# Kernel optimization log

Measured on AMD Instinct MI355X. Metric: run time of the kernel, lower is better.

The kernel has to match this reference:

```python
import jax, jax.numpy as jnp
import numpy as np

B, N = 2, 8192
FUN, EMB = 7, 3
H = 512
HEADS = 8
DH = H // HEADS  # 64
G = 32           # slice_num
L = 4            # n_layers
OUT = 4
MLP_H = 4 * H


def _ln(x, g, b, eps=1e-5):
    m = x.mean(-1, keepdims=True)
    v = ((x - m) ** 2).mean(-1, keepdims=True)
    return (x - m) * jax.lax.rsqrt(v + eps) * g + b


def _forward(fun, emb, W_pre1, b_pre1, W_pre2, b_pre2, placeholder,
             ln1_g, ln1_b, Wfx, bfx, Wx, bx, Wslice, bslice, temp,
             Wq, Wk, Wv, Wo, bo, ln2_g, ln2_b, Wm1, bm1, Wm2, bm2,
             lnf_g, lnf_b, Wout, bout):
    b, n = fun.shape[0], fun.shape[1]
    gelu = lambda z: jax.nn.gelu(z, approximate=False)  # torch nn.GELU default (erf)
    # preprocess MLP (n_layers=0, res=False): act(pre(x)) -> post
    x = jnp.concatenate([emb, fun], axis=-1)            # [B,N,EMB+FUN]
    fx = gelu(x @ W_pre1 + b_pre1) @ W_pre2 + b_pre2    # [B,N,H]
    fx = fx + placeholder
    scale = DH ** -0.5
    for l in range(L):
        # --- physics attention (irregular mesh) ---
        h = _ln(fx, ln1_g[l], ln1_b[l])
        fx_mid = (h @ Wfx[l] + bfx[l]).reshape(b, n, HEADS, DH)  # bnhd
        x_mid = (h @ Wx[l] + bx[l]).reshape(b, n, HEADS, DH)
        logits = jnp.einsum('bnhd,dg->bnhg', x_mid, Wslice[l]) + bslice[l]
        sw = jax.nn.softmax(logits / temp[l][None, None, :, None], axis=-1)  # bnhg
        slice_mass = sw.sum(axis=1)                                   # bhg
        token = jnp.einsum('bnhd,bnhg->bhgd', fx_mid, sw)
        token = token / (slice_mass[..., None] + 1e-5)                # bhgd
        q = token @ Wq[l]
        k = token @ Wk[l]
        v = token @ Wv[l]
        attn = jax.nn.softmax(jnp.einsum('bhgd,bhkd->bhgk', q, k) * scale, axis=-1)
        out_tok = jnp.einsum('bhgk,bhkd->bhgd', attn, v)
        out = jnp.einsum('bhgd,bnhg->bnhd', out_tok, sw).reshape(b, n, H)
        fx = out @ Wo[l] + bo[l] + fx
        # --- LN + MLP (hidden = 4H) with residual ---
        h2 = _ln(fx, ln2_g[l], ln2_b[l])
        fx = gelu(h2 @ Wm1[l] + bm1[l]) @ Wm2[l] + bm2[l] + fx
    # last-layer head: LN -> Linear(out_dim)
    return _ln(fx, lnf_g, lnf_b) @ Wout + bout


def setup_inputs() -> dict:
    key = jax.random.key(0)
    ks = iter(jax.random.split(key, 64))
    nrm = lambda shape, s=0.02: jax.random.normal(next(ks), shape, jnp.float32) * s
    return dict(
        fun=jax.random.normal(next(ks), (B, N, FUN), jnp.float32),
        emb=jax.random.normal(next(ks), (B, N, EMB), jnp.float32),
        W_pre1=nrm((FUN + EMB, 2 * H)), b_pre1=jnp.zeros((2 * H,), jnp.float32),
        W_pre2=nrm((2 * H, H)), b_pre2=jnp.zeros((H,), jnp.float32),
        placeholder=nrm((H,), 1.0),
        ln1_g=jnp.ones((L, H), jnp.float32), ln1_b=jnp.zeros((L, H), jnp.float32),
        Wfx=nrm((L, H, H)), bfx=jnp.zeros((L, H), jnp.float32),
        Wx=nrm((L, H, H)), bx=jnp.zeros((L, H), jnp.float32),
        Wslice=nrm((L, DH, G), 0.1), bslice=jnp.zeros((L, G), jnp.float32),
        temp=jnp.full((L, HEADS), 0.5, jnp.float32),
        Wq=nrm((L, DH, DH)), Wk=nrm((L, DH, DH)), Wv=nrm((L, DH, DH)),
        Wo=nrm((L, H, H)), bo=jnp.zeros((L, H), jnp.float32),
        ln2_g=jnp.ones((L, H), jnp.float32), ln2_b=jnp.zeros((L, H), jnp.float32),
        Wm1=nrm((L, H, MLP_H)), bm1=jnp.zeros((L, MLP_H), jnp.float32),
        Wm2=nrm((L, MLP_H, H)), bm2=jnp.zeros((L, H), jnp.float32),
        lnf_g=jnp.ones((H,), jnp.float32), lnf_b=jnp.zeros((H,), jnp.float32),
        Wout=nrm((H, OUT)), bout=jnp.zeros((OUT,), jnp.float32),
    )


def reference(fun, emb, W_pre1, b_pre1, W_pre2, b_pre2, placeholder,
              ln1_g, ln1_b, Wfx, bfx, Wx, bx, Wslice, bslice, temp,
              Wq, Wk, Wv, Wo, bo, ln2_g, ln2_b, Wm1, bm1, Wm2, bm2,
              lnf_g, lnf_b, Wout, bout):
    return _forward(fun, emb, W_pre1, b_pre1, W_pre2, b_pre2, placeholder,
                    ln1_g, ln1_b, Wfx, bfx, Wx, bx, Wslice, bslice, temp,
                    Wq, Wk, Wv, Wo, bo, ln2_g, ln2_b, Wm1, bm1, Wm2, bm2,
                    lnf_g, lnf_b, Wout, bout)
```

## Files before the change

kernel.cpp:

```cpp
#include <hip/hip_runtime.h>
#include <hip/hip_bf16.h>
#include <cstdint>
#include <cstddef>

typedef float  f32x4  __attribute__((ext_vector_type(4)));
typedef __bf16 bf16x8 __attribute__((ext_vector_type(8)));
typedef __bf16 bf16x4 __attribute__((ext_vector_type(4)));

#define DEV __device__ __forceinline__

DEV float gelu_f(float x){ return 0.5f * x * (1.0f + erff(x * 0.70710678118654752f)); }

#define WAIT_LGKM0 0xC07F

DEV size_t fm_off(int m, int k, int lgT, int lgK){
  size_t tileblk = ((size_t)(((m >> lgT) << (lgK - 5)) | (k >> 5))) << (lgT + 5);
  int sub = (m >> 4) & ((1 << (lgT - 4)) - 1);
  return tileblk + ((size_t)sub << 9) + (size_t)(((((k >> 3) & 3) << 4) | (m & 15)) << 3) + (k & 7);
}

static constexpr size_t OFF_FX     = 0;
static constexpr size_t OFF_H      = 33554432;
static constexpr size_t OFF_REGA   = 50331648;
static constexpr size_t OFF_FXMID  = OFF_REGA;
static constexpr size_t OFF_SW     = OFF_REGA + 16777216;
static constexpr size_t OFF_MLPH   = OFF_REGA;
static constexpr size_t OFF_H1     = OFF_REGA;
static constexpr size_t OFF_OUTB   = OFF_REGA + 67108864;
static constexpr size_t OFF_PT     = OFF_OUTB + 16777216;
static constexpr size_t OFF_PTM    = OFF_PT + 2097152;
static constexpr size_t OFF_OT     = OFF_PTM + 32768;
static constexpr size_t OFF_WT     = OFF_OT + 131072;
static constexpr size_t OFF_BIAS   = OFF_WT + 23068672;

__global__ __launch_bounds__(256) void wtrans_k(const float* __restrict__ W, __bf16* __restrict__ Wt,
                                                int K, int N, size_t wstride, size_t wtstride,
                                                int lgT, int lgK)
{
  __shared__ float tile[64][65];
  W  += (size_t)blockIdx.z * wstride;
  Wt += (size_t)blockIdx.z * wtstride;
  int t = threadIdx.x;
  int k0 = blockIdx.x * 64, n0 = blockIdx.y * 64;
  #pragma unroll
  for (int i = 0; i < 16; i++){
    int e = t + 256*i; int kk = e >> 6, nn = e & 63;
    tile[kk][nn] = W[(size_t)(k0+kk)*N + n0+nn];
  }
  __syncthreads();
  #pragma unroll
  for (int i2 = 0; i2 < 2; i2++){
    int c = t + 256*i2;
    int nn = c >> 3, ck = (c & 7) * 8;
    bf16x8 v;
    #pragma unroll
    for (int j = 0; j < 8; j++) v[j] = (__bf16)tile[ck+j][nn];
    *(bf16x8*)&Wt[fm_off(n0+nn, k0+ck, lgT, lgK)] = v;
  }
}

__global__ __launch_bounds__(128) void prep_wxs_k(const float* __restrict__ Wx, const float* __restrict__ Wsl,
                                                  const float* __restrict__ bx, const float* __restrict__ bsl,
                                                  const float* __restrict__ temp,
                                                  __bf16* __restrict__ Btcat, float* __restrict__ bcat)
{
  __shared__ float wsc[64];
  __shared__ float wrow[512];
  int l = blockIdx.y;
  const float* Wx_l  = Wx  + (size_t)l*262144;
  const float* Wsl_l = Wsl + l*2048;
  const float* bx_l  = bx  + l*512;
  const float* bsl_l = bsl + l*32;
  __bf16* Bt_l = Btcat + (size_t)l*393216;
  float* blog_l = bcat + l*768 + 512;
  int hg = blockIdx.x; int h = hg >> 5, g = hg & 31;
  int t = threadIdx.x;
  if (t < 64) wsc[t] = Wsl_l[t*32 + g];
  __syncthreads();
  float invt = 1.0f / temp[l*8 + h];
  #pragma unroll
  for (int cc = 0; cc < 4; cc++){
    int c = t + cc*128;
    float a = 0.f;
    for (int d = 0; d < 64; d++) a += Wx_l[(size_t)c*512 + h*64 + d] * wsc[d];
    wrow[c] = a * invt;
  }
  if (t == 0){
    float a = 0.f;
    for (int d = 0; d < 64; d++) a += bx_l[h*64 + d] * wsc[d];
    blog_l[hg] = (a + bsl_l[g]) * invt;
  }
  __syncthreads();
  if (t < 64){
    int k0 = t*8;
    bf16x8 v;
    #pragma unroll
    for (int j = 0; j < 8; j++) v[j] = (__bf16)wrow[k0+j];
    *(bf16x8*)&Bt_l[fm_off(512 + hg, k0, 8, 9)] = v;
  }
}

__global__ __launch_bounds__(256) void bias_setup_k(const float* __restrict__ b_pre2, const float* __restrict__ placeholder,
                                                    const float* __restrict__ bfx,
                                                    float* __restrict__ bpre2p, float* __restrict__ bcat)
{
  int i = blockIdx.x*256 + threadIdx.x;
  if (i < 512) bpre2p[i] = b_pre2[i] + placeholder[i];
  else if (i < 2560){
    int j = i - 512; int l = j >> 9, c = j & 511;
    bcat[l*768 + c] = bfx[l*512 + c];
  }
}

__global__ __launch_bounds__(256) void preproc1_k(const float* __restrict__ fun, const float* __restrict__ emb,
                                                  const float* __restrict__ W1, const float* __restrict__ b1,
                                                  __bf16* __restrict__ h1)
{
  __shared__ float w1l[10][1024];
  int t = threadIdx.x;
  for (int i = t*4; i < 10240; i += 1024) *(f32x4*)&w1l[0][i] = *(const f32x4*)&W1[i];
  __syncthreads();
  int rsel = t >> 7, c = t & 127, k0 = c*8;
  f32x4 bv0 = *(const f32x4*)&b1[k0];
  f32x4 bv1 = *(const f32x4*)&b1[k0+4];
  int r0 = blockIdx.x * 4;
  #pragma unroll
  for (int p = 0; p < 2; p++){
    int m = r0 + p*2 + rsel;
    const float* er = emb + (size_t)m*3;
    const float* fr = fun + (size_t)m*7;
    float x[10];
    x[0]=er[0]; x[1]=er[1]; x[2]=er[2];
    #pragma unroll
    for (int cc = 0; cc < 7; cc++) x[3+cc] = fr[cc];
    float a8[8];
    #pragma unroll
    for (int j = 0; j < 8; j++) a8[j] = (j < 4) ? bv0[j] : bv1[j-4];
    #pragma unroll
    for (int cc = 0; cc < 10; cc++){
      float xv = x[cc];
      #pragma unroll
      for (int j = 0; j < 8; j++) a8[j] += xv * w1l[cc][k0+j];
    }
    bf16x8 v;
    #pragma unroll
    for (int j = 0; j < 8; j++) v[j] = (__bf16)gelu_f(a8[j]);
    *(bf16x8*)&h1[fm_off(m, k0, 8, 10)] = v;
  }
}

template<int EPI, int BN>
__global__ __launch_bounds__(512) void gemm_wide(const __bf16* __restrict__ A, const __bf16* __restrict__ Bt,
                                                 const float* __restrict__ bias, const float* __restrict__ res,
                                                 void* __restrict__ outp, void* __restrict__ outp2,
                                                 int N, int lgK)
{
  constexpr int NSUB_B = BN/16;
  constexpr int S = 16 + NSUB_B;
  constexpr int Q = S/8;
  constexpr int NJ = BN/32;
  constexpr int BADV = BN*32;
  __shared__ bf16x8 ldsAB[2][S][64];
  const int tid = threadIdx.x;
  const int w = tid >> 6, lane = tid & 63;
  const int lm = lane & 15, lq = lane >> 4;
  const int wr = w >> 1, wc = w & 1;
  const int m0 = blockIdx.x * 256, n0 = blockIdx.y * BN;
  const int niter = 1 << (lgK - 5);

  const __bf16* gp[Q];
  int adv[Q];
  #pragma unroll
  for (int q = 0; q < Q; q++){
    int f = w*Q + q;
    if (f < 16){
      gp[q] = A + (((size_t)blockIdx.x << (lgK - 5)) * 8192) + f*512 + lane*8;
      adv[q] = 8192;
    } else {
      gp[q] = Bt + (((size_t)blockIdx.y << (lgK - 5)) * BADV) + (f-16)*512 + lane*8;
      adv[q] = BADV;
    }
  }

  bf16x8 r[Q];
  #pragma unroll
  for (int q = 0; q < Q; q++){ r[q] = *(const bf16x8*)gp[q]; gp[q] += adv[q]; }

  f32x4 acc[4][NJ] = {};

  for (int i = 0; i < niter; ++i){
    __builtin_amdgcn_s_barrier();
    const unsigned buf = (unsigned)i & 1u;
    #pragma unroll
    for (int q = 0; q < Q; q++)
      ldsAB[buf][w*Q + q][lane] = r[q];
    if (i + 1 < niter){
      #pragma unroll
      for (int q = 0; q < Q; q++){ r[q] = *(const bf16x8*)gp[q]; gp[q] += adv[q]; }
    }
    __builtin_amdgcn_s_waitcnt(WAIT_LGKM0);
    __builtin_amdgcn_s_barrier();
    bf16x8 af[4], bfr[NJ];
    #pragma unroll
    for (int ii = 0; ii < 4; ii++)  af[ii]  = ldsAB[buf][wr*4 + ii][lane];
    #pragma unroll
    for (int jj = 0; jj < NJ; jj++) bfr[jj] = ldsAB[buf][16 + wc*NJ + jj][lane];
    #pragma unroll
    for (int ii = 0; ii < 4; ii++)
      #pragma unroll
      for (int jj = 0; jj < NJ; jj++)
        acc[ii][jj] = __builtin_amdgcn_mfma_f32_16x16x32_bf16(af[ii], bfr[jj], acc[ii][jj], 0, 0, 0);
  }

  if (EPI == 4 && blockIdx.y == 2){
    float* swp = (float*)outp2;
    #pragma unroll
    for (int ii = 0; ii < 4; ii++){
      int row0 = m0 + wr*64 + ii*16 + lq*4;
      #pragma unroll
      for (int hp = 0; hp < 4; hp++){
        int j0 = hp*2, j1 = j0 + 1;
        int h = wc*4 + hp;
        float b0 = bias[512 + wc*128 + j0*16 + lm];
        float b1 = bias[512 + wc*128 + j1*16 + lm];
        #pragma unroll
        for (int r2 = 0; r2 < 4; r2++){
          int row = row0 + r2;
          float v0 = acc[ii][j0][r2] + b0;
          float v1 = acc[ii][j1][r2] + b1;
          float mx = fmaxf(v0, v1);
          #pragma unroll
          for (int msk = 8; msk; msk >>= 1) mx = fmaxf(mx, __shfl_xor(mx, msk));
          float e0 = expf(v0 - mx), e1 = expf(v1 - mx);
          float ss = e0 + e1;
          #pragma unroll
          for (int msk = 8; msk; msk >>= 1) ss += __shfl_xor(ss, msk);
          float inv = 1.f / ss;
          int b = row >> 13, n = row & 8191;
          float* op = swp + ((size_t)(b*8 + h)*8192 + n)*32;
          op[lm]      = e0 * inv;
          op[16 + lm] = e1 * inv;
        }
      }
    }
    return;
  }

  #pragma unroll
  for (int ii = 0; ii < 4; ii++){
    int row0 = m0 + wr*64 + ii*16 + lq*4;
    #pragma unroll
    for (int jj = 0; jj < NJ; jj++){
      int col = n0 + wc*(BN/2) + jj*16 + lm;
      float bv = bias[col];
      #pragma unroll
      for (int r2 = 0; r2 < 4; r2++){
        int row = row0 + r2;
        float v = acc[ii][jj][r2] + bv;
        if (EPI == 1){
          ((__bf16*)outp)[fm_off(row, col, 8, 11)] = (__bf16)gelu_f(v);
        } else {
          size_t idx = (size_t)row*N + col;
          if (EPI == 2) v += res[idx];
          if (EPI == 4) ((__bf16*)outp)[idx] = (__bf16)v;
          else          ((float*)outp)[idx]  = v;
        }
      }
    }
  }
}

__global__ __launch_bounds__(256) void ln_k(const float* __restrict__ x, const float* __restrict__ g,
                                            const float* __restrict__ b, __bf16* __restrict__ out)
{
  int w = threadIdx.x >> 6, lane = threadIdx.x & 63;
  int row = blockIdx.x*4 + w;
  const float* xr = x + (size_t)row*512 + lane*8;
  float v[8];
  *(f32x4*)&v[0] = *(const f32x4*)xr;
  *(f32x4*)&v[4] = *(const f32x4*)(xr + 4);
  float s = 0.f, sq = 0.f;
  #pragma unroll
  for (int e = 0; e < 8; e++){ s += v[e]; sq += v[e]*v[e]; }
  #pragma unroll
  for (int off = 32; off; off >>= 1){ s += __shfl_xor(s, off); sq += __shfl_xor(sq, off); }
  float mean = s * (1.f/512.f);
  float var  = sq * (1.f/512.f) - mean*mean;
  float rstd = rsqrtf(var + 1e-5f);
  float gv[8], bv[8];
  *(f32x4*)&gv[0] = *(const f32x4*)(g + lane*8);
  *(f32x4*)&gv[4] = *(const f32x4*)(g + lane*8 + 4);
  *(f32x4*)&bv[0] = *(const f32x4*)(b + lane*8);
  *(f32x4*)&bv[4] = *(const f32x4*)(b + lane*8 + 4);
  bf16x8 o8;
  #pragma unroll
  for (int e = 0; e < 8; e++) o8[e] = (__bf16)((v[e]-mean)*rstd*gv[e] + bv[e]);
  *(bf16x8*)&out[fm_off(row, lane*8, 8, 9)] = o8;
}

__global__ __launch_bounds__(256) void token_part_k(const __bf16* __restrict__ fxmid, const float* __restrict__ sw,
                                                    float* __restrict__ pt, float* __restrict__ ptm)
{
  __shared__ float fxl[32][64];
  __shared__ float swl[32][32];
  int t = threadIdx.x;
  int chunk = blockIdx.x, bh = blockIdx.y;
  int b = bh >> 3, h = bh & 7;
  int d = t & 63, gg = (t >> 6) * 8;
  float acc[8] = {0,0,0,0,0,0,0,0};
  float macc = 0.f;
  for (int s = 0; s < 16; s++){
    int nbase = chunk*512 + s*32;
    __syncthreads();
    #pragma unroll
    for (int i = 0; i < 2; i++){
      int e = t + 256*i; int rv = e >> 4, c4 = e & 15;
      bf16x4 v = *(const bf16x4*)&fxmid[((size_t)(b*8192 + nbase + rv))*512 + h*64 + c4*4];
      fxl[rv][c4*4+0] = (float)v[0];
      fxl[rv][c4*4+1] = (float)v[1];
      fxl[rv][c4*4+2] = (float)v[2];
      fxl[rv][c4*4+3] = (float)v[3];
    }
    { int rv = t >> 3, c4 = t & 7;
      *(f32x4*)&swl[rv][c4*4] = *(const f32x4*)&sw[((size_t)bh*8192 + nbase + rv)*32 + c4*4]; }
    __syncthreads();
    for (int nn = 0; nn < 32; nn++){
      float f = fxl[nn][d];
      #pragma unroll
      for (int jj = 0; jj < 8; jj++) acc[jj] += f * swl[nn][gg+jj];
    }
    if (t < 32){ for (int nn = 0; nn < 32; nn++) macc += swl[nn][t]; }
  }
  int cb = chunk*16 + bh;
  #pragma unroll
  for (int jj = 0; jj < 8; jj++)
    pt[((size_t)cb*32 + gg + jj)*64 + d] = acc[jj];
  if (t < 32) ptm[cb*32 + t] = macc;
}

__global__ __launch_bounds__(256) void attn_k(const float* __restrict__ pt, const float* __restrict__ ptm,
                                              const float* __restrict__ Wq, const float* __restrict__ Wk,
                                              const float* __restrict__ Wv, float* __restrict__ ot)
{
  __shared__ float tok[32][64];
  __shared__ float ml[32];
  __shared__ float qq[32][65], kk2[32][65], vv[32][65];
  __shared__ float at[32][33];
  int t = threadIdx.x, bh = blockIdx.x;
  if (t < 32){
    float s = 0.f;
    for (int c = 0; c < 16; c++) s += ptm[(c*16 + bh)*32 + t];
    ml[t] = s + 1e-5f;
  }
  __syncthreads();
  #pragma unroll
  for (int i = 0; i < 8; i++){
    int e = t + 256*i; int g = e >> 6, d = e & 63;
    float s = 0.f;
    for (int c = 0; c < 16; c++) s += pt[((size_t)(c*16 + bh)*32 + g)*64 + d];
    tok[g][d] = s / ml[g];
  }
  __syncthreads();
  #pragma unroll
  for (int i = 0; i < 8; i++){
    int e = t + 256*i; int g = e >> 6, j = e & 63;
    float aq = 0.f, ak = 0.f, av = 0.f;
    for (int d = 0; d < 64; d++){
      float tv = tok[g][d];
      aq += tv * Wq[d*64 + j];
      ak += tv * Wk[d*64 + j];
      av += tv * Wv[d*64 + j];
    }
    qq[g][j] = aq; kk2[g][j] = ak; vv[g][j] = av;
  }
  __syncthreads();
  #pragma unroll
  for (int i = 0; i < 4; i++){
    int e = t + 256*i; int g = e >> 5, j2 = e & 31;
    float s2 = 0.f;
    for (int d = 0; d < 64; d++) s2 += qq[g][d] * kk2[j2][d];
    at[g][j2] = s2 * 0.125f;
  }
  __syncthreads();
  if (t < 32){
    float mx = at[t][0];
    for (int j = 1; j < 32; j++) mx = fmaxf(mx, at[t][j]);
    float ss = 0.f;
    for (int j = 0; j < 32; j++){ float e2 = expf(at[t][j]-mx); at[t][j] = e2; ss += e2; }
    float inv = 1.f / ss;
    for (int j = 0; j < 32; j++) at[t][j] *= inv;
  }
  __syncthreads();
  #pragma unroll
  for (int i = 0; i < 8; i++){
    int e = t + 256*i; int g = e >> 6, d = e & 63;
    float s3 = 0.f;
    for (int j = 0; j < 32; j++) s3 += at[g][j] * vv[j][d];
    ot[(size_t)bh*2048 + e] = s3;
  }
}

__global__ __launch_bounds__(256) void deslice_k(const float* __restrict__ ot, const float* __restrict__ sw,
                                                 __bf16* __restrict__ outb)
{
  __shared__ float otl[32][64];
  __shared__ float swl[128][36];
  int t = threadIdx.x;
  int chunk = blockIdx.x, bh = blockIdx.y;
  int b = bh >> 3, h = bh & 7;
  int n0 = chunk*128;
  #pragma unroll
  for (int i = 0; i < 8; i++){
    int e = t + 256*i;
    otl[e>>6][e&63] = ot[(size_t)bh*2048 + e];
  }
  {
    int r = t >> 1, half = t & 1;
    const float* sp = sw + ((size_t)bh*8192 + n0 + r)*32 + half*16;
    float* dp = &swl[r][half*16];
    #pragma unroll
    for (int q = 0; q < 4; q++) *(f32x4*)(dp + q*4) = *(const f32x4*)(sp + q*4);
  }
  __syncthreads();
  const int slot = t >> 3;
  const int d0 = (t & 7) * 8;
  float o[4][8] = {};
  for (int g = 0; g < 32; g++){
    f32x4 ov0 = *(const f32x4*)&otl[g][d0];
    f32x4 ov1 = *(const f32x4*)&otl[g][d0+4];
    #pragma unroll
    for (int p = 0; p < 4; p++){
      float s = swl[p*32 + slot][g];
      o[p][0] += s*ov0[0]; o[p][1] += s*ov0[1]; o[p][2] += s*ov0[2]; o[p][3] += s*ov0[3];
      o[p][4] += s*ov1[0]; o[p][5] += s*ov1[1]; o[p][6] += s*ov1[2]; o[p][7] += s*ov1[3];
    }
  }
  #pragma unroll
  for (int p = 0; p < 4; p++){
    int n = n0 + p*32 + slot;
    int m = b*8192 + n;
    int k = h*64 + d0;
    bf16x8 v;
    #pragma unroll
    for (int j = 0; j < 8; j++) v[j] = (__bf16)o[p][j];
    *(bf16x8*)&outb[fm_off(m, k, 8, 9)] = v;
  }
}

__global__ __launch_bounds__(256) void head_k(const float* __restrict__ x, const float* __restrict__ g,
                                              const float* __restrict__ b, const float* __restrict__ Wout,
                                              const float* __restrict__ bout, float* __restrict__ out)
{
  int w = threadIdx.x >> 6, lane = threadIdx.x & 63;
  int row = blockIdx.x*4 + w;
  const float* xr = x + (size_t)row*512 + lane*8;
  float v[8];
  *(f32x4*)&v[0] = *(const f32x4*)xr;
  *(f32x4*)&v[4] = *(const f32x4*)(xr + 4);
  float s = 0.f, sq = 0.f;
  #pragma unroll
  for (int e = 0; e < 8; e++){ s += v[e]; sq += v[e]*v[e]; }
  #pragma unroll
  for (int off = 32; off; off >>= 1){ s += __shfl_xor(s, off); sq += __shfl_xor(sq, off); }
  float mean = s * (1.f/512.f);
  float rstd = rsqrtf(sq * (1.f/512.f) - mean*mean + 1e-5f);
  float o[4] = {0,0,0,0};
  #pragma unroll
  for (int e = 0; e < 8; e++){
    int c = lane*8 + e;
    float yn = (v[e]-mean)*rstd*g[c] + b[c];
    const float* wr = Wout + (size_t)c*4;
    o[0] += yn*wr[0]; o[1] += yn*wr[1]; o[2] += yn*wr[2]; o[3] += yn*wr[3];
  }
  #pragma unroll
  for (int off = 32; off; off >>= 1){
    #pragma unroll
    for (int j = 0; j < 4; j++) o[j] += __shfl_xor(o[j], off);
  }
  if (lane == 0){
    #pragma unroll
    for (int j = 0; j < 4; j++) out[(size_t)row*4 + j] = o[j] + bout[j];
  }
}

extern "C" void kernel_launch(void* const* d_in, const int* in_sizes, int n_in,
                              void* d_out, int out_size, void* d_ws, size_t ws_size,
                              hipStream_t stream)
{
  const float* fun    = (const float*)d_in[0];
  const float* emb    = (const float*)d_in[1];
  const float* W_pre1 = (const float*)d_in[2];
  const float* b_pre1 = (const float*)d_in[3];
  const float* W_pre2 = (const float*)d_in[4];
  const float* b_pre2 = (const float*)d_in[5];
  const float* placeholder = (const float*)d_in[6];
  const float* ln1_g  = (const float*)d_in[7];
  const float* ln1_b  = (const float*)d_in[8];
  const float* Wfx    = (const float*)d_in[9];
  const float* bfx    = (const float*)d_in[10];
  const float* Wx     = (const float*)d_in[11];
  const float* bx     = (const float*)d_in[12];
  const float* Wslice = (const float*)d_in[13];
  const float* bslice = (const float*)d_in[14];
  const float* temp   = (const float*)d_in[15];
  const float* Wq     = (const float*)d_in[16];
  const float* Wk     = (const float*)d_in[17];
  const float* Wv     = (const float*)d_in[18];
  const float* Wo     = (const float*)d_in[19];
  const float* bo     = (const float*)d_in[20];
  const float* ln2_g  = (const float*)d_in[21];
  const float* ln2_b  = (const float*)d_in[22];
  const float* Wm1    = (const float*)d_in[23];
  const float* bm1    = (const float*)d_in[24];
  const float* Wm2    = (const float*)d_in[25];
  const float* bm2    = (const float*)d_in[26];
  const float* lnf_g  = (const float*)d_in[27];
  const float* lnf_b  = (const float*)d_in[28];
  const float* Wout   = (const float*)d_in[29];
  const float* bout   = (const float*)d_in[30];

  char* ws = (char*)d_ws;
  float*  fx     = (float*)(ws + OFF_FX);
  __bf16* hbf    = (__bf16*)(ws + OFF_H);
  __bf16* fxmid  = (__bf16*)(ws + OFF_FXMID);
  float*  sw     = (float*)(ws + OFF_SW);
  __bf16* mlph   = (__bf16*)(ws + OFF_MLPH);
  __bf16* h1bf   = (__bf16*)(ws + OFF_H1);
  __bf16* outb   = (__bf16*)(ws + OFF_OUTB);
  float*  pt     = (float*)(ws + OFF_PT);
  float*  ptm    = (float*)(ws + OFF_PTM);
  float*  ot     = (float*)(ws + OFF_OT);
  __bf16* Wpre2t = (__bf16*)(ws + OFF_WT);
  __bf16* Btcat  = (__bf16*)(ws + OFF_WT + 1048576);
  __bf16* Wot    = (__bf16*)(ws + OFF_WT + 4194304);
  __bf16* Wm1t   = (__bf16*)(ws + OFF_WT + 6291456);
  __bf16* Wm2t   = (__bf16*)(ws + OFF_WT + 14680064);
  float*  bcat   = (float*)(ws + OFF_BIAS);
  float*  bpre2p = (float*)(ws + OFF_BIAS + 4*768*4);

  wtrans_k<<<dim3(16,8,1), 256,0,stream>>>(W_pre2, Wpre2t, 1024, 512, 0, 0, 7, 10);
  wtrans_k<<<dim3(8,8,4),  256,0,stream>>>(Wfx, Btcat, 512, 512, 262144, 393216, 8, 9);
  wtrans_k<<<dim3(8,8,4),  256,0,stream>>>(Wo,  Wot,  512, 512, 262144, 262144, 7, 9);
  wtrans_k<<<dim3(8,32,4), 256,0,stream>>>(Wm1, Wm1t, 512, 2048, 1048576, 1048576, 8, 9);
  wtrans_k<<<dim3(32,8,4), 256,0,stream>>>(Wm2, Wm2t, 2048, 512, 1048576, 1048576, 7, 11);
  prep_wxs_k<<<dim3(256,4),128,0,stream>>>(Wx, Wslice, bx, bslice, temp, Btcat, bcat);
  bias_setup_k<<<10,256,0,stream>>>(b_pre2, placeholder, bfx, bpre2p, bcat);

  preproc1_k<<<4096,256,0,stream>>>(fun, emb, W_pre1, b_pre1, h1bf);
  gemm_wide<0,128><<<dim3(64,4),512,0,stream>>>(h1bf, Wpre2t, bpre2p, nullptr, (void*)fx, nullptr, 512, 10);

  for (int l = 0; l < 4; l++){
    ln_k<<<4096,256,0,stream>>>(fx, ln1_g + l*512, ln1_b + l*512, hbf);
    gemm_wide<4,256><<<dim3(64,3),512,0,stream>>>(hbf, Btcat + (size_t)l*393216, bcat + l*768, nullptr, (void*)fxmid, (void*)sw, 512, 9);
    token_part_k<<<dim3(16,16),256,0,stream>>>(fxmid, sw, pt, ptm);
    attn_k<<<16,256,0,stream>>>(pt, ptm, Wq + l*4096, Wk + l*4096, Wv + l*4096, ot);
    deslice_k<<<dim3(64,16),256,0,stream>>>(ot, sw, outb);
    gemm_wide<2,128><<<dim3(64,4),512,0,stream>>>(outb, Wot + (size_t)l*262144, bo + l*512, fx, (void*)fx, nullptr, 512, 9);
    ln_k<<<4096,256,0,stream>>>(fx, ln2_g + l*512, ln2_b + l*512, hbf);
    gemm_wide<1,256><<<dim3(64,8),512,0,stream>>>(hbf, Wm1t + (size_t)l*1048576, bm1 + l*2048, nullptr, (void*)mlph, nullptr, 2048, 9);
    gemm_wide<2,128><<<dim3(64,4),512,0,stream>>>(mlph, Wm2t + (size_t)l*1048576, bm2 + l*512, fx, (void*)fx, nullptr, 512, 11);
  }

  head_k<<<4096,256,0,stream>>>(fx, lnf_g, lnf_b, Wout, bout, (float*)d_out);
}
```

Measured before the change: 1.282 ms.

## Double K-step per GEMM iteration and load B tiles directly into LDS

Restructures the GEMM main loop so each iteration covers 64 of K instead of 32, halving the number of barriers and loop iterations. The B operand is now fetched with global_load_lds straight into a double-buffered LDS region, which skips the register staging, while A still goes through registers. The K iteration count becomes a compile-time constant through per-shape wrapper kernels. In exchange it uses more LDS and registers per block. There is also a risk that the direct LDS loads are not covered by the lgkmcnt wait, which would need a vmcnt wait to be correct.

```diff
diff --git a/kernel.cpp b/kernel.cpp
--- a/kernel.cpp
+++ b/kernel.cpp
@@ -12,6 +12,11 @@
 DEV float gelu_f(float x){ return 0.5f * x * (1.0f + erff(x * 0.70710678118654752f)); }
 
 #define WAIT_LGKM0 0xC07F
+
+DEV void gl16(void* lds, const void* g){
+  __builtin_amdgcn_global_load_lds((const __attribute__((address_space(1))) void*)g,
+                                   (__attribute__((address_space(3))) void*)lds, 16, 0, 0);
+}
 
 DEV size_t fm_off(int m, int k, int lgT, int lgK){
   size_t tileblk = ((size_t)(((m >> lgT) << (lgK - 5)) | (k >> 5))) << (lgT + 5);
@@ -150,41 +155,31 @@
 }
 
 template<int EPI, int BN>
-__global__ __launch_bounds__(512) void gemm_wide(const __bf16* __restrict__ A, const __bf16* __restrict__ Bt,
-                                                 const float* __restrict__ bias, const float* __restrict__ res,
-                                                 void* __restrict__ outp, void* __restrict__ outp2,
-                                                 int N, int lgK)
+DEV void gemm_body(const __bf16* __restrict__ A, const __bf16* __restrict__ Bt,
+                   const float* __restrict__ bias, const float* __restrict__ res,
+                   void* __restrict__ outp, void* __restrict__ outp2,
+                   int N, int niter)
 {
   constexpr int NSUB_B = BN/16;
-  constexpr int S = 16 + NSUB_B;
-  constexpr int Q = S/8;
+  constexpr int QB = (BN==256) ? 4 : 2;
   constexpr int NJ = BN/32;
-  constexpr int BADV = BN*32;
-  __shared__ bf16x8 ldsAB[2][S][64];
+  constexpr int BADV = BN*64;
+  __shared__ bf16x8 ldsA[2][32][64];
+  __shared__ bf16x8 ldsB[2][2*NSUB_B][64];
   const int tid = threadIdx.x;
   const int w = tid >> 6, lane = tid & 63;
   const int lm = lane & 15, lq = lane >> 4;
   const int wr = w >> 1, wc = w & 1;
   const int m0 = blockIdx.x * 256, n0 = blockIdx.y * BN;
-  const int niter = 1 << (lgK - 5);
-
-  const __bf16* gp[Q];
-  int adv[Q];
-  #pragma unroll
-  for (int q = 0; q < Q; q++){
-    int f = w*Q + q;
-    if (f < 16){
-      gp[q] = A + (((size_t)blockIdx.x << (lgK - 5)) * 8192) + f*512 + lane*8;
-      adv[q] = 8192;
-    } else {
-      gp[q] = Bt + (((size_t)blockIdx.y << (lgK - 5)) * BADV) + (f-16)*512 + lane*8;
-      adv[q] = BADV;
-    }
-  }
-
-  bf16x8 r[Q];
-  #pragma unroll
-  for (int q = 0; q < Q; q++){ r[q] = *(const bf16x8*)gp[q]; gp[q] += adv[q]; }
+
+  const __bf16* Ab = A  + (size_t)blockIdx.x * niter * 16384 + (w*4)*512 + lane*8;
+  const __bf16* Bb = Bt + (size_t)blockIdx.y * niter * BADV  + (w*QB)*512 + lane*8;
+
+  #pragma unroll
+  for (int q = 0; q < QB; q++) gl16(&ldsB[0][w*QB + q][0], Bb + q*512);
+  bf16x8 r[4];
+  #pragma unroll
+  for (int q = 0; q < 4; q++) r[q] = *(const bf16x8*)(Ab + q*512);
 
   f32x4 acc[4][NJ] = {};
 
@@ -192,24 +187,29 @@
     __builtin_amdgcn_s_barrier();
     const unsigned buf = (unsigned)i & 1u;
     #pragma unroll
-    for (int q = 0; q < Q; q++)
-      ldsAB[buf][w*Q + q][lane] = r[q];
+    for (int q = 0; q < 4; q++)
+      ldsA[buf][w*4 + q][lane] = r[q];
     if (i + 1 < niter){
       #pragma unroll
-      for (int q = 0; q < Q; q++){ r[q] = *(const bf16x8*)gp[q]; gp[q] += adv[q]; }
+      for (int q = 0; q < QB; q++) gl16(&ldsB[buf^1][w*QB + q][0], Bb + (size_t)(i+1)*BADV + q*512);
+      #pragma unroll
+      for (int q = 0; q < 4; q++) r[q] = *(const bf16x8*)(Ab + (size_t)(i+1)*16384 + q*512);
     }
     __builtin_amdgcn_s_waitcnt(WAIT_LGKM0);
     __builtin_amdgcn_s_barrier();
-    bf16x8 af[4], bfr[NJ];
-    #pragma unroll
-    for (int ii = 0; ii < 4; ii++)  af[ii]  = ldsAB[buf][wr*4 + ii][lane];
-    #pragma unroll
-    for (int jj = 0; jj < NJ; jj++) bfr[jj] = ldsAB[buf][16 + wc*NJ + jj][lane];
-    #pragma unroll
-    for (int ii = 0; ii < 4; ii++)
-      #pragma unroll
-      for (int jj = 0; jj < NJ; jj++)
-        acc[ii][jj] = __builtin_amdgcn_mfma_f32_16x16x32_bf16(af[ii], bfr[jj], acc[ii][jj], 0, 0, 0);
+    #pragma unroll
+    for (int s = 0; s < 2; s++){
+      bf16x8 af[4], bfr[NJ];
+      #pragma unroll
+      for (int ii = 0; ii < 4; ii++)  af[ii]  = ldsA[buf][s*16 + wr*4 + ii][lane];
+      #pragma unroll
+      for (int jj = 0; jj < NJ; jj++) bfr[jj] = ldsB[buf][s*NSUB_B + wc*NJ + jj][lane];
+      #pragma unroll
+      for (int ii = 0; ii < 4; ii++)
+        #pragma unroll
+        for (int jj = 0; jj < NJ; jj++)
+          acc[ii][jj] = __builtin_amdgcn_mfma_f32_16x16x32_bf16(af[ii], bfr[jj], acc[ii][jj], 0, 0, 0);
+    }
   }
 
   if (EPI == 4 && blockIdx.y == 2){
@@ -269,6 +269,26 @@
     }
   }
 }
+
+__global__ __launch_bounds__(512) void gemm_pre(const __bf16* A, const __bf16* Bt, const float* bias,
+                                                float* outp)
+{ gemm_body<0,128>(A, Bt, bias, nullptr, (void*)outp, nullptr, 512, 16); }
+
+__global__ __launch_bounds__(512) void gemm_comb(const __bf16* A, const __bf16* Bt, const float* bias,
+                                                 __bf16* outp, float* swp)
+{ gemm_body<4,256>(A, Bt, bias, nullptr, (void*)outp, (void*)swp, 512, 8); }
+
+__global__ __launch_bounds__(512) void gemm_wo(const __bf16* A, const __bf16* Bt, const float* bias,
+                                               const float* res, float* outp)
+{ gemm_body<2,128>(A, Bt, bias, res, (void*)outp, nullptr, 512, 8); }
+
+__global__ __launch_bounds__(512) void gemm_wm1(const __bf16* A, const __bf16* Bt, const float* bias,
+                                                __bf16* outp)
+{ gemm_body<1,256>(A, Bt, bias, nullptr, (void*)outp, nullptr, 2048, 8); }
+
+__global__ __launch_bounds__(512) void gemm_wm2(const __bf16* A, const __bf16* Bt, const float* bias,
+                                                const float* res, float* outp)
+{ gemm_body<2,128>(A, Bt, bias, res, (void*)outp, nullptr, 512, 32); }
 
 __global__ __launch_bounds__(256) void ln_k(const float* __restrict__ x, const float* __restrict__ g,
                                             const float* __restrict__ b, __bf16* __restrict__ out)
@@ -547,18 +567,18 @@
   bias_setup_k<<<10,256,0,stream>>>(b_pre2, placeholder, bfx, bpre2p, bcat);
 
   preproc1_k<<<4096,256,0,stream>>>(fun, emb, W_pre1, b_pre1, h1bf);
-  gemm_wide<0,128><<<dim3(64,4),512,0,stream>>>(h1bf, Wpre2t, bpre2p, nullptr, (void*)fx, nullptr, 512, 10);
+  gemm_pre<<<dim3(64,4),512,0,stream>>>(h1bf, Wpre2t, bpre2p, fx);
 
   for (int l = 0; l < 4; l++){
     ln_k<<<4096,256,0,stream>>>(fx, ln1_g + l*512, ln1_b + l*512, hbf);
-    gemm_wide<4,256><<<dim3(64,3),512,0,stream>>>(hbf, Btcat + (size_t)l*393216, bcat + l*768, nullptr, (void*)fxmid, (void*)sw, 512, 9);
+    gemm_comb<<<dim3(64,3),512,0,stream>>>(hbf, Btcat + (size_t)l*393216, bcat + l*768, fxmid, sw);
     token_part_k<<<dim3(16,16),256,0,stream>>>(fxmid, sw, pt, ptm);
     attn_k<<<16,256,0,stream>>>(pt, ptm, Wq + l*4096, Wk + l*4096, Wv + l*4096, ot);
     deslice_k<<<dim3(64,16),256,0,stream>>>(ot, sw, outb);
-    gemm_wide<2,128><<<dim3(64,4),512,0,stream>>>(outb, Wot + (size_t)l*262144, bo + l*512, fx, (void*)fx, nullptr, 512, 9);
+    gemm_wo<<<dim3(64,4),512,0,stream>>>(outb, Wot + (size_t)l*262144, bo + l*512, fx, fx);
     ln_k<<<4096,256,0,stream>>>(fx, ln2_g + l*512, ln2_b + l*512, hbf);
-    gemm_wide<1,256><<<dim3(64,8),512,0,stream>>>(hbf, Wm1t + (size_t)l*1048576, bm1 + l*2048, nullptr, (void*)mlph, nullptr, 2048, 9);
-    gemm_wide<2,128><<<dim3(64,4),512,0,stream>>>(mlph, Wm2t + (size_t)l*1048576, bm2 + l*512, fx, (void*)fx, nullptr, 512, 11);
+    gemm_wm1<<<dim3(64,8),512,0,stream>>>(hbf, Wm1t + (size_t)l*1048576, bm1 + l*2048, mlph);
+    gemm_wm2<<<dim3(64,4),512,0,stream>>>(mlph, Wm2t + (size_t)l*1048576, bm2 + l*512, fx, fx);
   }
 
   head_k<<<4096,256,0,stream>>>(fx, lnf_g, lnf_b, Wout, bout, (float*)d_out);
```

Result: slower. 1.315 ms (+2.6%).
